# Optimization experiments

Measured on AMD Instinct MI355X. Metric: run time of the kernel, lower is better.

## Reference

```python
import jax, jax.numpy as jnp
import numpy as np
from jax import lax

PAD = 20          # pad_size == max_displacement
MAX_DISP = 20
STRIDE2 = 2
D = 2 * MAX_DISP // STRIDE2 + 1  # 21 displacement positions per axis -> 441 channels


def setup_inputs() -> dict:
    key = jax.random.key(0)
    k1, k2 = jax.random.split(key)
    B, C, H, W = 16, 256, 64, 96
    input1 = jax.random.normal(k1, (B, C, H, W), dtype=jnp.float32)
    input2 = jax.random.normal(k2, (B, C, H, W), dtype=jnp.float32)
    return {"input1": input1, "input2": input2}


def _correlation(f1, f2):
    # FlowNet correlation: kernel_size=1, stride1=1, pad_size==max_displacement.
    # out[b, dy*D+dx, y, x] = (1/C) * sum_c f1[b,c,y,x] * f2_padded[b,c,y+dy*s2, x+dx*s2]
    B, C, H, W = f1.shape
    f2p = jnp.pad(f2, ((0, 0), (0, 0), (PAD, PAD), (PAD, PAD)))
    # all (dy, dx) pixel offsets into the padded map
    ii, jj = jnp.meshgrid(jnp.arange(D) * STRIDE2, jnp.arange(D) * STRIDE2, indexing="ij")
    offsets = jnp.stack([ii.reshape(-1), jj.reshape(-1)], axis=-1)  # [D*D, 2]

    def step(carry, off):
        dy, dx = off[0], off[1]
        sl = lax.dynamic_slice(f2p, (0, 0, dy, dx), (B, C, H, W))
        corr = jnp.einsum("bchw,bchw->bhw", f1, sl)  # channel dot product
        return carry, corr

    _, maps = lax.scan(step, None, offsets)  # [D*D, B, H, W]
    out = jnp.transpose(maps, (1, 0, 2, 3)) / jnp.float32(C)
    return out  # [B, D*D, H, W]


def reference(input1, input2):
    return _correlation(input1, input2)
```

## Files before the change

### kernel.cpp

```cpp
#include <hip/hip_runtime.h>

typedef _Float16 half8 __attribute__((ext_vector_type(8)));
typedef float floatx4 __attribute__((ext_vector_type(4)));

constexpr int Bn = 16, Cn = 256, Hn = 64, Wn = 96;
constexpr int HW = Hn * Wn;
constexpr int Dn = 21, ND = Dn * Dn;
constexpr int PH = Hn + 40;
constexpr int PW = Wn + 40;
constexpr int PHW = PH * PW;
constexpr int TY = 8, TX = 32;
constexpr int NTY = Hn / TY;
constexpr int NTX = Wn / TX;
constexpr int NJ = (TX + 40) / 2;
constexpr int GP = 506;
constexpr int SMEM_BYTES = 129536;
constexpr size_t QB_STRIDE  = (size_t)PH * 68 * 64;
constexpr size_t KS_STRIDE  = 2 * QB_STRIDE;
constexpr size_t B2_STRIDE  = 8 * KS_STRIDE;

constexpr size_t F1T_BYTES = (size_t)Bn * HW * Cn * 2;
constexpr size_t F2T_BYTES = (size_t)Bn * B2_STRIDE;
constexpr size_t WS_NEEDED = F1T_BYTES + F2T_BYTES;

constexpr int F1_BLKS = Bn * (HW / 64);
constexpr int F2_BLKS = Bn * (PHW / 64);

__global__ __launch_bounds__(256)
void tconv_all(const float* __restrict__ f1, const float* __restrict__ f2,
               _Float16* __restrict__ f1t, _Float16* __restrict__ f2t2) {
  int blk = blockIdx.x;
  const int t = threadIdx.x;
  const int pxl = t >> 2;
  const int g = t & 3;
  if (blk < F1_BLKS) {
    const int b = blk / (HW / 64);
    const int px = (blk % (HW / 64)) * 64 + pxl;
    const float* src = f1 + (size_t)b * Cn * HW + px;
    _Float16* dst = f1t + ((size_t)b * HW + px) * Cn;
#pragma unroll
    for (int it = 0; it < 8; ++it) {
      const int c0 = (g + it * 4) * 8;
      half8 v;
#pragma unroll
      for (int k = 0; k < 8; ++k)
        v[k] = (_Float16)src[(size_t)(c0 + k) * HW];
      *(half8*)(dst + c0) = v;
    }
  } else {
    blk -= F1_BLKS;
    const int b = blk / (PHW / 64);
    const int ppx = (blk % (PHW / 64)) * 64 + pxl;
    const int py = ppx / PW;
    const int px = ppx - py * PW;
    const int qb = px & 1;
    const int cx = px >> 1;
    const int yy = py - 20, xx = px - 20;
    const bool valid = (yy >= 0) & (yy < Hn) & (xx >= 0) & (xx < Wn);
    const float* src = f2 + (size_t)b * Cn * HW + (valid ? (yy * Wn + xx) : 0);
#pragma unroll
    for (int h = 0; h < 2; ++h) {
      const int ks = g + h * 4;
      _Float16* dst = (_Float16*)((char*)f2t2 + (size_t)b * B2_STRIDE
                                  + (size_t)ks * KS_STRIDE + (size_t)qb * QB_STRIDE
                                  + ((size_t)py * 68 + cx) * 64);
#pragma unroll
      for (int q = 0; q < 4; ++q) {
        half8 v;
#pragma unroll
        for (int k = 0; k < 8; ++k) {
          const float f = src[(size_t)(ks * 32 + q * 8 + k) * HW];
          v[k] = (_Float16)(valid ? f : 0.0f);
        }
        *(half8*)(dst + q * 8) = v;
      }
    }
  }
}

#define GLLDS(gp, lo) \
  __builtin_amdgcn_global_load_lds( \
      (const __attribute__((address_space(1))) void*)(gp), \
      (__attribute__((address_space(3))) void*)(uintptr_t)(lo), 16, 0, 0)
#define DSREAD(dst, addr, OFFSTR) \
  asm volatile("ds_read_b128 %0, %1 offset:" OFFSTR : "=v"(dst) : "v"(addr));

__global__ __launch_bounds__(512, 2)
void corr15(const _Float16* __restrict__ f1t, const _Float16* __restrict__ f2t2,
            float* __restrict__ out) {
  __shared__ __align__(16) char SMEM[SMEM_BYTES];

  int bid = (int)blockIdx.x;
  bid = (bid & 7) * 192 + (bid >> 3);
  const int tx = bid % NTX;
  int tmp = bid / NTX;
  const int ty = tmp % NTY;
  tmp /= NTY;
  const int qa = tmp & 1;
  tmp >>= 1;
  const int chunk = tmp & 1;
  const int b = tmp >> 1;
  const int y0 = ty * TY, x0 = tx * TX;

  const int r = chunk ? 10 : 11;
  const int dyLo = chunk ? 11 : 0;
  const int rows = r + 3;
  const int NNc = rows * NJ;
  const int ndch = r * Dn;

  const int t = threadIdx.x;
  const int lane = t & 63;
  const int wave = t >> 6;
  const int l15 = lane & 15;
  const int lk = lane >> 4;
  const int qbR = wave >> 2;
  const int w4 = wave & 3;

  const _Float16* f1b = f1t + (size_t)b * HW * Cn;
  const char* f2base = (const char*)f2t2 + (size_t)b * B2_STRIDE
                       + (size_t)qbR * QB_STRIDE;
  const float invc = 1.0f / 256.0f;

  const unsigned wdest = __builtin_amdgcn_readfirstlane((unsigned)(wave * 8192));

  unsigned soff[8];
#pragma unroll
  for (int u = 0; u < 8; ++u) {
    int s = w4 * 128 + u * 16 + (lane >> 2);
    if (s >= NNc) s = 0;
    const int q = ((lane & 3) - (s >> 1)) & 3;
    const int row = s / NJ, col = s % NJ;
    const int py = y0 + qa + 2 * (row + dyLo);
    soff[u] = (unsigned)(((py * 68 + (x0 >> 1) + col) * 64) + q * 16);
  }

  const int p = (lk + ((l15 >> 1) & 3)) & 3;
  const unsigned ra = wdest + (unsigned)(l15 * 64 + p * 16);

  const _Float16* ap0 = f1b + (size_t)((y0 + qa + 0) * Wn + x0 + qbR + 2 * l15) * Cn + lk * 8;
  const _Float16* ap1 = ap0 + (size_t)2 * Wn * Cn;
  const _Float16* ap2 = ap0 + (size_t)4 * Wn * Cn;
  const _Float16* ap3 = ap0 + (size_t)6 * Wn * Cn;

  floatx4 acc[4][8];
#pragma unroll
  for (int m = 0; m < 4; ++m)
#pragma unroll
    for (int i = 0; i < 8; ++i)
      acc[m][i] = {0.f, 0.f, 0.f, 0.f};
  half8 aA0, aA1, aA2, aA3, aB0, aB1, aB2, aB3;

  auto ISSUE = [&](int h, half8& A0, half8& A1, half8& A2, half8& A3) {
    const int sc = h >> 1, gg = h & 1;
    const char* f2s = f2base + (size_t)sc * KS_STRIDE;
#pragma unroll
    for (int k = 0; k < 4; ++k)
      GLLDS(f2s + soff[gg * 4 + k], wdest + (unsigned)(gg * 4096 + k * 1024));
    if (gg == 0) {
      const int kb = sc * 64;
      asm volatile("global_load_dwordx4 %0, %1, off" : "=v"(A0) : "v"((const char*)ap0 + kb));
      asm volatile("global_load_dwordx4 %0, %1, off" : "=v"(A1) : "v"((const char*)ap1 + kb));
      asm volatile("global_load_dwordx4 %0, %1, off" : "=v"(A2) : "v"((const char*)ap2 + kb));
      asm volatile("global_load_dwordx4 %0, %1, off" : "=v"(A3) : "v"((const char*)ap3 + kb));
    }
  };
  auto COMPUTE = [&](int h, const half8& A0, const half8& A1,
                     const half8& A2, const half8& A3) {
    const int gg = h & 1;
    half8 bf[4];
    if (gg == 0) {
      DSREAD(bf[0], ra, "0")    DSREAD(bf[1], ra, "1024")
      DSREAD(bf[2], ra, "2048") DSREAD(bf[3], ra, "3072")
    } else {
      DSREAD(bf[0], ra, "4096") DSREAD(bf[1], ra, "5120")
      DSREAD(bf[2], ra, "6144") DSREAD(bf[3], ra, "7168")
    }
    asm volatile("s_waitcnt lgkmcnt(0)");
    __builtin_amdgcn_sched_barrier(0);
#pragma unroll
    for (int k = 0; k < 4; ++k) {
      const int ti = gg * 4 + k;
      acc[0][ti] = __builtin_amdgcn_mfma_f32_16x16x32_f16(A0, bf[k], acc[0][ti], 0, 0, 0);
      acc[1][ti] = __builtin_amdgcn_mfma_f32_16x16x32_f16(A1, bf[k], acc[1][ti], 0, 0, 0);
      acc[2][ti] = __builtin_amdgcn_mfma_f32_16x16x32_f16(A2, bf[k], acc[2][ti], 0, 0, 0);
      acc[3][ti] = __builtin_amdgcn_mfma_f32_16x16x32_f16(A3, bf[k], acc[3][ti], 0, 0, 0);
    }
  };

  ISSUE(0, aA0, aA1, aA2, aA3);
  ISSUE(1, aA0, aA1, aA2, aA3);
#pragma unroll
  for (int h = 0; h < 16; ++h) {
    if (h == 15)     { asm volatile("s_waitcnt vmcnt(0)" ::: "memory"); }
    else if (h & 1)  { asm volatile("s_waitcnt vmcnt(8)" ::: "memory"); }
    else             { asm volatile("s_waitcnt vmcnt(4)" ::: "memory"); }
    __builtin_amdgcn_sched_barrier(0);
    if (((h >> 1) & 1) == 0) COMPUTE(h, aA0, aA1, aA2, aA3);
    else                     COMPUTE(h, aB0, aB1, aB2, aB3);
    if (h + 2 < 16) {
      if ((((h + 2) >> 1) & 1) == 0) ISSUE(h + 2, aA0, aA1, aA2, aA3);
      else                           ISSUE(h + 2, aB0, aB1, aB2, aB3);
    }
  }
  __syncthreads();

  _Float16* const Gh = (_Float16*)SMEM;
#pragma unroll
  for (int mt = 0; mt < 4; ++mt) {
#pragma unroll
    for (int ti = 0; ti < 8; ++ti) {
      const int n = w4 * 128 + ti * 16 + l15;
      if (n < NNc) {
#pragma unroll
        for (int rr = 0; rr < 4; ++rr)
          Gh[(qbR * 64 + mt * 16 + lk * 4 + rr) * GP + n] =
              (_Float16)(acc[mt][ti][rr] * invc);
      }
    }
  }
  __syncthreads();

  {
    const int niter = (ndch + 15) >> 4;
    const int dsub = t >> 5;
    const int alpha = (t >> 3) & 3;
    const int xq = t & 7;
    const int yy = y0 + qa + 2 * alpha;
    float* ob = out + (size_t)b * ND * HW + yy * Wn + x0 + xq * 4;
    const int m0 = alpha * 16 + xq * 2;
    for (int q = 0; q < niter; ++q) {
      const int dch = q * 16 + dsub;
      if (dch < ndch) {
        const unsigned dyl = (unsigned)dch / 21u;
        const int dx = dch - (int)dyl * 21;
        const int dy = dyLo + (int)dyl;
        const int col = ((int)dyl + alpha) * NJ + xq * 2 + dx;
        floatx4 v;
        v[0] = (float)Gh[(m0) * GP + col];
        v[1] = (float)Gh[(64 + m0) * GP + col];
        v[2] = (float)Gh[(m0 + 1) * GP + col + 1];
        v[3] = (float)Gh[(64 + m0 + 1) * GP + col + 1];
        __builtin_nontemporal_store(v, (floatx4*)(ob + (size_t)(dy * Dn + dx) * HW));
      }
    }
  }
}

constexpr int FTY = 8, FTX = 8;
constexpr int FNTY = Hn / FTY, FNTX = Wn / FTX;
constexpr int FNJ = 24, FNTILES = 36, FGP = 580;

__global__ __launch_bounds__(256, 4)
void corr_fallback(const float* __restrict__ f1, const float* __restrict__ f2,
                   float* __restrict__ out) {
  __shared__ float G[16 * FGP];
  const int bid = blockIdx.x;
  const int cls = bid & 3;
  const int t2 = bid >> 2;
  const int tx = t2 % FNTX;
  const int t3 = t2 / FNTX;
  const int ty = t3 % FNTY;
  const int b = t3 / FNTY;
  const int qa = cls >> 1, qb = cls & 1;
  const int y0 = ty * FTY, x0 = tx * FTX;
  const int lane = threadIdx.x & 63;
  const int wave = threadIdx.x >> 6;
  const int l15 = lane & 15;
  const int lk = lane >> 4;
  const float* f1b = f1 + b * (Cn * HW);
  const float* f2b = f2 + b * (Cn * HW);
  const int ay = y0 + qa + 2 * (l15 >> 2);
  const int ax = x0 + qb + 2 * (l15 & 3);
  const float* f1p = f1b + ay * Wn + ax;
  half8 afrag[8];
#pragma unroll
  for (int ks = 0; ks < 8; ++ks)
#pragma unroll
    for (int tt = 0; tt < 8; ++tt)
      afrag[ks][tt] = (_Float16)f1p[(ks * 32 + lk * 8 + tt) * HW];
  const int nt0 = wave * (FNTILES / 4);
  for (int nt = nt0; nt < nt0 + FNTILES / 4; ++nt) {
    const unsigned n = nt * 16 + l15;
    const int i = n / (unsigned)FNJ;
    const int j = n % (unsigned)FNJ;
    const int y2 = y0 - 20 + qa + 2 * i;
    const int x2 = x0 - 20 + qb + 2 * j;
    const bool inb = (y2 >= 0) & (y2 < Hn) & (x2 >= 0) & (x2 < Wn);
    const float* f2p = f2b + (inb ? (y2 * Wn + x2) : 0);
    floatx4 acc = {0.f, 0.f, 0.f, 0.f};
#pragma unroll
    for (int ks = 0; ks < 8; ++ks) {
      half8 bfrag;
#pragma unroll
      for (int tt = 0; tt < 8; ++tt) {
        const float v = f2p[(ks * 32 + lk * 8 + tt) * HW];
        bfrag[tt] = (_Float16)(inb ? v : 0.0f);
      }
      acc = __builtin_amdgcn_mfma_f32_16x16x32_f16(afrag[ks], bfrag, acc, 0, 0, 0);
    }
#pragma unroll
    for (int r = 0; r < 4; ++r)
      G[(4 * lk + r) * FGP + n] = acc[r];
  }
  __syncthreads();
  float* outb = out + b * (ND * HW);
  const float invc = 1.0f / 256.0f;
  for (int o = threadIdx.x; o < ND * 16; o += 256) {
    const int d = o >> 4;
    const int m = o & 15;
    const int dy = (unsigned)d / 21u;
    const int dx = (unsigned)d % 21u;
    const int alpha = m >> 2, beta = m & 3;
    const float val = G[m * FGP + (alpha + dy) * FNJ + (beta + dx)] * invc;
    outb[d * HW + (y0 + qa + 2 * alpha) * Wn + (x0 + qb + 2 * beta)] = val;
  }
}

extern "C" void kernel_launch(void* const* d_in, const int* in_sizes, int n_in,
                              void* d_out, int out_size, void* d_ws, size_t ws_size,
                              hipStream_t stream) {
  const float* f1 = (const float*)d_in[0];
  const float* f2 = (const float*)d_in[1];
  float* out = (float*)d_out;
  if (ws_size >= WS_NEEDED) {
    _Float16* f1t = (_Float16*)d_ws;
    _Float16* f2t2 = (_Float16*)((char*)d_ws + F1T_BYTES);
    tconv_all<<<dim3(F1_BLKS + F2_BLKS), dim3(256), 0, stream>>>(f1, f2, f1t, f2t2);
    corr15<<<dim3(Bn * 2 * NTY * NTX * 2), dim3(512), 0, stream>>>(f1t, f2t2, out);
  } else {
    corr_fallback<<<dim3(Bn * FNTY * FNTX * 4), dim3(256), 0, stream>>>(f1, f2, out);
  }
}
```

Baseline: 217.3 us.

## Read f1 directly as fp32 in correlation kernel, drop f1 transpose pass

Removes the f1 transpose/fp16-conversion pre-pass and has the correlation kernel load f1 straight from the NCHW fp32 input with scalar dword loads, converting to fp16 in registers before the MFMAs. This eliminates writing and re-reading an fp16 copy of f1 (roughly 50MB of traffic) and shrinks the prep kernel. In exchange each wave issues 32 scalar loads per k-step instead of 4 vector loads, strided by channel, which raises register pressure and vmcnt bookkeeping, and f1 may be re-read from memory by the two chunk blocks.

```diff
diff --git a/kernel.cpp b/kernel.cpp
--- a/kernel.cpp
+++ b/kernel.cpp
@@ -19,61 +19,41 @@
 constexpr size_t KS_STRIDE  = 2 * QB_STRIDE;
 constexpr size_t B2_STRIDE  = 8 * KS_STRIDE;
 
-constexpr size_t F1T_BYTES = (size_t)Bn * HW * Cn * 2;
 constexpr size_t F2T_BYTES = (size_t)Bn * B2_STRIDE;
-constexpr size_t WS_NEEDED = F1T_BYTES + F2T_BYTES;
-
-constexpr int F1_BLKS = Bn * (HW / 64);
+constexpr size_t WS_NEEDED = F2T_BYTES;
+
 constexpr int F2_BLKS = Bn * (PHW / 64);
 
 __global__ __launch_bounds__(256)
-void tconv_all(const float* __restrict__ f1, const float* __restrict__ f2,
-               _Float16* __restrict__ f1t, _Float16* __restrict__ f2t2) {
-  int blk = blockIdx.x;
+void tconv_f2(const float* __restrict__ f2, _Float16* __restrict__ f2t2) {
+  const int blk = blockIdx.x;
   const int t = threadIdx.x;
   const int pxl = t >> 2;
   const int g = t & 3;
-  if (blk < F1_BLKS) {
-    const int b = blk / (HW / 64);
-    const int px = (blk % (HW / 64)) * 64 + pxl;
-    const float* src = f1 + (size_t)b * Cn * HW + px;
-    _Float16* dst = f1t + ((size_t)b * HW + px) * Cn;
-#pragma unroll
-    for (int it = 0; it < 8; ++it) {
-      const int c0 = (g + it * 4) * 8;
+  const int b = blk / (PHW / 64);
+  const int ppx = (blk % (PHW / 64)) * 64 + pxl;
+  const int py = ppx / PW;
+  const int px = ppx - py * PW;
+  const int qb = px & 1;
+  const int cx = px >> 1;
+  const int yy = py - 20, xx = px - 20;
+  const bool valid = (yy >= 0) & (yy < Hn) & (xx >= 0) & (xx < Wn);
+  const float* src = f2 + (size_t)b * Cn * HW + (valid ? (yy * Wn + xx) : 0);
+#pragma unroll
+  for (int h = 0; h < 2; ++h) {
+    const int ks = g + h * 4;
+    _Float16* dst = (_Float16*)((char*)f2t2 + (size_t)b * B2_STRIDE
+                                + (size_t)ks * KS_STRIDE + (size_t)qb * QB_STRIDE
+                                + ((size_t)py * 68 + cx) * 64);
+#pragma unroll
+    for (int q = 0; q < 4; ++q) {
       half8 v;
 #pragma unroll
-      for (int k = 0; k < 8; ++k)
-        v[k] = (_Float16)src[(size_t)(c0 + k) * HW];
-      *(half8*)(dst + c0) = v;
-    }
-  } else {
-    blk -= F1_BLKS;
-    const int b = blk / (PHW / 64);
-    const int ppx = (blk % (PHW / 64)) * 64 + pxl;
-    const int py = ppx / PW;
-    const int px = ppx - py * PW;
-    const int qb = px & 1;
-    const int cx = px >> 1;
-    const int yy = py - 20, xx = px - 20;
-    const bool valid = (yy >= 0) & (yy < Hn) & (xx >= 0) & (xx < Wn);
-    const float* src = f2 + (size_t)b * Cn * HW + (valid ? (yy * Wn + xx) : 0);
-#pragma unroll
-    for (int h = 0; h < 2; ++h) {
-      const int ks = g + h * 4;
-      _Float16* dst = (_Float16*)((char*)f2t2 + (size_t)b * B2_STRIDE
-                                  + (size_t)ks * KS_STRIDE + (size_t)qb * QB_STRIDE
-                                  + ((size_t)py * 68 + cx) * 64);
-#pragma unroll
-      for (int q = 0; q < 4; ++q) {
-        half8 v;
-#pragma unroll
-        for (int k = 0; k < 8; ++k) {
-          const float f = src[(size_t)(ks * 32 + q * 8 + k) * HW];
-          v[k] = (_Float16)(valid ? f : 0.0f);
-        }
-        *(half8*)(dst + q * 8) = v;
-      }
+      for (int k = 0; k < 8; ++k) {
+        const float f = src[(size_t)(ks * 32 + q * 8 + k) * HW];
+        v[k] = (_Float16)(valid ? f : 0.0f);
+      }
+      *(half8*)(dst + q * 8) = v;
     }
   }
 }
@@ -84,9 +64,12 @@
       (__attribute__((address_space(3))) void*)(uintptr_t)(lo), 16, 0, 0)
 #define DSREAD(dst, addr, OFFSTR) \
   asm volatile("ds_read_b128 %0, %1 offset:" OFFSTR : "=v"(dst) : "v"(addr));
+#define GLD(dst, voff, sb, OFFSTR) \
+  asm volatile("global_load_dword %0, %1, %2 offset:" OFFSTR \
+               : "=v"(dst) : "v"(voff), "s"(sb));
 
 __global__ __launch_bounds__(512, 2)
-void corr15(const _Float16* __restrict__ f1t, const _Float16* __restrict__ f2t2,
+void corr17(const float* __restrict__ f1, const _Float16* __restrict__ f2t2,
             float* __restrict__ out) {
   __shared__ __align__(16) char SMEM[SMEM_BYTES];
 
@@ -116,9 +99,9 @@
   const int qbR = wave >> 2;
   const int w4 = wave & 3;
 
-  const _Float16* f1b = f1t + (size_t)b * HW * Cn;
   const char* f2base = (const char*)f2t2 + (size_t)b * B2_STRIDE
                        + (size_t)qbR * QB_STRIDE;
+  const float* f1b = f1 + (size_t)b * Cn * HW;
   const float invc = 1.0f / 256.0f;
 
   const unsigned wdest = __builtin_amdgcn_readfirstlane((unsigned)(wave * 8192));
@@ -137,10 +120,14 @@
   const int p = (lk + ((l15 >> 1) & 3)) & 3;
   const unsigned ra = wdest + (unsigned)(l15 * 64 + p * 16);
 
-  const _Float16* ap0 = f1b + (size_t)((y0 + qa + 0) * Wn + x0 + qbR + 2 * l15) * Cn + lk * 8;
-  const _Float16* ap1 = ap0 + (size_t)2 * Wn * Cn;
-  const _Float16* ap2 = ap0 + (size_t)4 * Wn * Cn;
-  const _Float16* ap3 = ap0 + (size_t)6 * Wn * Cn;
+  unsigned voff[8];
+  {
+    const unsigned pix = (unsigned)(((y0 + qa) * Wn + x0 + qbR + 2 * l15) * 4);
+#pragma unroll
+    for (int k = 0; k < 8; ++k)
+      voff[k] = pix + (unsigned)((lk * 8 + k) * HW * 4);
+  }
+  constexpr unsigned KSTEPB = 32u * HW * 4u;
 
   floatx4 acc[4][8];
 #pragma unroll
@@ -148,25 +135,40 @@
 #pragma unroll
     for (int i = 0; i < 8; ++i)
       acc[m][i] = {0.f, 0.f, 0.f, 0.f};
-  half8 aA0, aA1, aA2, aA3, aB0, aB1, aB2, aB3;
-
-  auto ISSUE = [&](int h, half8& A0, half8& A1, half8& A2, half8& A3) {
+  float Araw[2][4][8];
+  half8 Afh[4];
+
+  auto ISSUE = [&](int h) {
     const int sc = h >> 1, gg = h & 1;
     const char* f2s = f2base + (size_t)sc * KS_STRIDE;
 #pragma unroll
     for (int k = 0; k < 4; ++k)
       GLLDS(f2s + soff[gg * 4 + k], wdest + (unsigned)(gg * 4096 + k * 1024));
     if (gg == 0) {
-      const int kb = sc * 64;
-      asm volatile("global_load_dwordx4 %0, %1, off" : "=v"(A0) : "v"((const char*)ap0 + kb));
-      asm volatile("global_load_dwordx4 %0, %1, off" : "=v"(A1) : "v"((const char*)ap1 + kb));
-      asm volatile("global_load_dwordx4 %0, %1, off" : "=v"(A2) : "v"((const char*)ap2 + kb));
-      asm volatile("global_load_dwordx4 %0, %1, off" : "=v"(A3) : "v"((const char*)ap3 + kb));
+      const int as = sc & 1;
+#pragma unroll
+      for (int k = 0; k < 8; ++k) {
+        GLD(Araw[as][0][k], voff[k], f1b, "0")
+        GLD(Araw[as][1][k], voff[k], f1b, "768")
+        GLD(Araw[as][2][k], voff[k], f1b, "1536")
+        GLD(Araw[as][3][k], voff[k], f1b, "2304")
+        voff[k] += KSTEPB;
+      }
     }
   };
-  auto COMPUTE = [&](int h, const half8& A0, const half8& A1,
-                     const half8& A2, const half8& A3) {
+  auto COMPUTE = [&](int h) {
     const int gg = h & 1;
+    if (gg == 0) {
+      const int as = (h >> 1) & 1;
+#pragma unroll
+      for (int mt = 0; mt < 4; ++mt) {
+        half8 v;
+#pragma unroll
+        for (int k = 0; k < 8; ++k)
+          v[k] = (_Float16)Araw[as][mt][k];
+        Afh[mt] = v;
+      }
+    }
     half8 bf[4];
     if (gg == 0) {
       DSREAD(bf[0], ra, "0")    DSREAD(bf[1], ra, "1024")
@@ -180,27 +182,22 @@
 #pragma unroll
     for (int k = 0; k < 4; ++k) {
       const int ti = gg * 4 + k;
-      acc[0][ti] = __builtin_amdgcn_mfma_f32_16x16x32_f16(A0, bf[k], acc[0][ti], 0, 0, 0);
-      acc[1][ti] = __builtin_amdgcn_mfma_f32_16x16x32_f16(A1, bf[k], acc[1][ti], 0, 0, 0);
-      acc[2][ti] = __builtin_amdgcn_mfma_f32_16x16x32_f16(A2, bf[k], acc[2][ti], 0, 0, 0);
-      acc[3][ti] = __builtin_amdgcn_mfma_f32_16x16x32_f16(A3, bf[k], acc[3][ti], 0, 0, 0);
+      acc[0][ti] = __builtin_amdgcn_mfma_f32_16x16x32_f16(Afh[0], bf[k], acc[0][ti], 0, 0, 0);
+      acc[1][ti] = __builtin_amdgcn_mfma_f32_16x16x32_f16(Afh[1], bf[k], acc[1][ti], 0, 0, 0);
+      acc[2][ti] = __builtin_amdgcn_mfma_f32_16x16x32_f16(Afh[2], bf[k], acc[2][ti], 0, 0, 0);
+      acc[3][ti] = __builtin_amdgcn_mfma_f32_16x16x32_f16(Afh[3], bf[k], acc[3][ti], 0, 0, 0);
     }
   };
 
-  ISSUE(0, aA0, aA1, aA2, aA3);
-  ISSUE(1, aA0, aA1, aA2, aA3);
+  ISSUE(0); ISSUE(1);
 #pragma unroll
   for (int h = 0; h < 16; ++h) {
-    if (h == 15)     { asm volatile("s_waitcnt vmcnt(0)" ::: "memory"); }
-    else if (h & 1)  { asm volatile("s_waitcnt vmcnt(8)" ::: "memory"); }
-    else             { asm volatile("s_waitcnt vmcnt(4)" ::: "memory"); }
+    if (h == 15)     { asm volatile("s_waitcnt vmcnt(0)"  ::: "memory"); }
+    else if (h & 1)  { asm volatile("s_waitcnt vmcnt(36)" ::: "memory"); }
+    else             { asm volatile("s_waitcnt vmcnt(4)"  ::: "memory"); }
     __builtin_amdgcn_sched_barrier(0);
-    if (((h >> 1) & 1) == 0) COMPUTE(h, aA0, aA1, aA2, aA3);
-    else                     COMPUTE(h, aB0, aB1, aB2, aB3);
-    if (h + 2 < 16) {
-      if ((((h + 2) >> 1) & 1) == 0) ISSUE(h + 2, aA0, aA1, aA2, aA3);
-      else                           ISSUE(h + 2, aB0, aB1, aB2, aB3);
-    }
+    COMPUTE(h);
+    if (h + 2 < 16) ISSUE(h + 2);
   }
   __syncthreads();
 
@@ -323,10 +320,9 @@
   const float* f2 = (const float*)d_in[1];
   float* out = (float*)d_out;
   if (ws_size >= WS_NEEDED) {
-    _Float16* f1t = (_Float16*)d_ws;
-    _Float16* f2t2 = (_Float16*)((char*)d_ws + F1T_BYTES);
-    tconv_all<<<dim3(F1_BLKS + F2_BLKS), dim3(256), 0, stream>>>(f1, f2, f1t, f2t2);
-    corr15<<<dim3(Bn * 2 * NTY * NTX * 2), dim3(512), 0, stream>>>(f1t, f2t2, out);
+    _Float16* f2t2 = (_Float16*)d_ws;
+    tconv_f2<<<dim3(F2_BLKS), dim3(256), 0, stream>>>(f2, f2t2);
+    corr17<<<dim3(Bn * 2 * NTY * NTX * 2), dim3(512), 0, stream>>>(f1, f2t2, out);
   } else {
     corr_fallback<<<dim3(Bn * FNTY * FNTX * 4), dim3(256), 0, stream>>>(f1, f2, out);
   }
```

Result: slower. 250.0 us (+15.0%).
